# Kernel tuning notes

Hardware: AMD Instinct MI355X
Metric: run time of the kernel (lower is better)

The kernel has to match this reference:

```python
import jax, jax.numpy as jnp
import numpy as np

DIM = 768
N_HEADS = 12
HEAD_DIM = DIM // N_HEADS
SCALE = HEAD_DIM ** -0.5


def setup_inputs() -> dict:
    key = jax.random.key(0)
    kx, kqkv, kpw, kpb = jax.random.split(key, 4)
    B, N = 16, 1024
    x = jax.random.normal(kx, (B, N, DIM), dtype=jnp.float32)
    # nn.Linear weights stored [out, in]; torch computes x @ W.T + b
    w_qkv = jax.random.normal(kqkv, (3 * DIM, DIM), dtype=jnp.float32) * (DIM ** -0.5)
    w_proj = jax.random.normal(kpw, (DIM, DIM), dtype=jnp.float32) * (DIM ** -0.5)
    b_proj = jax.random.normal(kpb, (DIM,), dtype=jnp.float32) * 0.01
    return {"x": x, "w_qkv": w_qkv, "w_proj": w_proj, "b_proj": b_proj}


def reference(x, w_qkv, w_proj, b_proj):
    B, N, C = x.shape
    # qkv: [B, N, 3C] -> [3, B, H, N, Dh]
    qkv = (x @ w_qkv.T).reshape(B, N, 3, N_HEADS, HEAD_DIM)
    qkv = jnp.transpose(qkv, (2, 0, 3, 1, 4))
    q, k, v = qkv[0], qkv[1], qkv[2]
    # scores: [B, H, N, N]
    scores = jnp.einsum("bhnd,bhmd->bhnm", q, k) * SCALE
    attn = jax.nn.softmax(scores, axis=-1)
    out = jnp.einsum("bhnm,bhmd->bhnd", attn, v)
    out = jnp.transpose(out, (0, 2, 1, 3)).reshape(B, N, C)
    return out @ w_proj.T + b_proj
```

## Files before the change

kernel.cpp:

```cpp
#include <hip/hip_runtime.h>
#include <stdint.h>


typedef unsigned short u16;
typedef __attribute__((ext_vector_type(8))) short s16x8;
typedef __attribute__((ext_vector_type(4))) float f32x4;
typedef __attribute__((ext_vector_type(4))) unsigned short u16x4;

#define SEQ 1024
#define NHEAD 12
#define HD 64

__device__ __forceinline__ u16 f2bf(float f) {
  union { float f; uint32_t u; } v; v.f = f;
  uint32_t u = v.u;
  return (u16)((u + 0x7FFFu + ((u >> 16) & 1u)) >> 16);
}

__device__ __forceinline__ float exp2_fast(float x) {
  return __builtin_amdgcn_exp2f(x);
}

__device__ __forceinline__ uint32_t pk_bf16(float a, float b) {
#if __has_builtin(__builtin_amdgcn_cvt_pk_bf16_f32)
  typedef __attribute__((ext_vector_type(2))) __bf16 bf2;
  union { bf2 v; uint32_t u; } c;
  c.v = __builtin_amdgcn_cvt_pk_bf16_f32(a, b);
  return c.u;
#else
  union { float f; uint32_t u; } ua, ub; ua.f = a; ub.f = b;
  const uint32_t ra = ua.u + 0x8000u, rb = ub.u + 0x8000u;
  return __builtin_amdgcn_perm(ra, rb, 0x03020706u);
#endif
}

__device__ __forceinline__ void gld_lds16(const void* g, void* l) {
  __builtin_amdgcn_global_load_lds((const __attribute__((address_space(1))) void*)g,
                                   (__attribute__((address_space(3))) void*)l, 16, 0, 0);
}

__global__ void cvt_bf16(const float* __restrict__ in, u16* __restrict__ out, int n4) {
  int i = blockIdx.x * blockDim.x + threadIdx.x;
  if (i < n4) {
    float4 f = ((const float4*)in)[i];
    u16x4 o;
    o.x = f2bf(f.x); o.y = f2bf(f.y); o.z = f2bf(f.z); o.w = f2bf(f.w);
    ((u16x4*)out)[i] = o;
  }
}

template <int EPI>
__global__ __launch_bounds__(256, 3)
void gemm_bt(const u16* __restrict__ A, const u16* __restrict__ B,
             u16* __restrict__ q, u16* __restrict__ k, u16* __restrict__ v,
             float* __restrict__ out, const float* __restrict__ bias) {
  __shared__ u16 As[128 * 64];
  __shared__ u16 Bs[128 * 64];
  const int tid = threadIdx.x;
  const int wv = tid >> 6, lane = tid & 63;
  const int quad = lane >> 4, l16 = lane & 15;
  const int m0 = blockIdx.x * 128, n0 = blockIdx.y * 128;
  const int wm = (wv & 1) * 64, wn = (wv >> 1) * 64;

  f32x4 acc[4][4];
#pragma unroll
  for (int i = 0; i < 4; i++)
#pragma unroll
    for (int j = 0; j < 4; j++) { acc[i][j].x = 0.f; acc[i][j].y = 0.f; acc[i][j].z = 0.f; acc[i][j].w = 0.f; }

  const int srow = (lane >> 3);
  const int scp = lane & 7;

  for (int kt = 0; kt < 768; kt += 64) {
    __syncthreads();
#pragma unroll
    for (int i = 0; i < 4; i++) {
      const int t = wv * 4 + i;
      const int row = t * 8 + srow;
      const int c = scp ^ (row & 7);
      gld_lds16(A + (size_t)(m0 + row) * 768 + kt + c * 8, &As[t * 512]);
      gld_lds16(B + (size_t)(n0 + row) * 768 + kt + c * 8, &Bs[t * 512]);
    }
    __syncthreads();
#pragma unroll
    for (int ks = 0; ks < 2; ks++) {
      s16x8 af[4], bf[4];
#pragma unroll
      for (int mi = 0; mi < 4; mi++) {
        const int ra = wm + mi * 16 + l16;
        const int ca = ((ks * 4 + quad) ^ (ra & 7)) * 8;
        af[mi] = *(const s16x8*)&As[ra * 64 + ca];
        const int rb = wn + mi * 16 + l16;
        const int cb = ((ks * 4 + quad) ^ (rb & 7)) * 8;
        bf[mi] = *(const s16x8*)&Bs[rb * 64 + cb];
      }
#pragma unroll
      for (int mi = 0; mi < 4; mi++)
#pragma unroll
        for (int ni = 0; ni < 4; ni++)
          acc[mi][ni] = __builtin_amdgcn_mfma_f32_16x16x32_bf16(af[mi], bf[ni], acc[mi][ni], 0, 0, 0);
    }
  }

#pragma unroll
  for (int mi = 0; mi < 4; mi++) {
#pragma unroll
    for (int ni = 0; ni < 4; ni++) {
#pragma unroll
      for (int r = 0; r < 4; r++) {
        const int m = m0 + wm + mi * 16 + quad * 4 + r;
        const int n = n0 + wn + ni * 16 + l16;
        const float val = acc[mi][ni][r];
        if (EPI == 0) {
          const int which = n / 768;
          const int rc = n % 768;
          const int head = rc >> 6, d = rc & 63;
          const int b = m >> 10, rr = m & 1023;
          if (which == 0)
            q[((size_t)(b * NHEAD + head) * SEQ + rr) * HD + d] = f2bf(val * 0.18033688011112042f);
          else if (which == 1)
            k[((size_t)(b * NHEAD + head) * SEQ + rr) * HD + d] = f2bf(val);
          else
            v[((size_t)(b * NHEAD + head) * HD + d) * SEQ + rr] = f2bf(val);
        } else {
          out[(size_t)m * 768 + n] = val + bias[n];
        }
      }
    }
  }
}

__global__ __launch_bounds__(256, 3)
void flash_attn(const u16* __restrict__ Q, const u16* __restrict__ K,
                const u16* __restrict__ VT, u16* __restrict__ O) {
  __shared__ u16 Ks[2][64 * 64];
  __shared__ u16 Vs[2][64 * 64];
  __shared__ u16 Ps[4][32 * 64];

  const int tid = threadIdx.x;
  const int wv = tid >> 6, lane = tid & 63;
  const int quad = lane >> 4, l16 = lane & 15;
  const int bh = blockIdx.x;
  const int q0 = blockIdx.y * 128 + wv * 32;
  const size_t base = (size_t)bh * SEQ * HD;
  const size_t vbase = (size_t)bh * HD * SEQ;
  u16* pw = Ps[wv];

  const int sr0 = tid >> 3;
  const int sc0 = (tid & 7) ^ (sr0 & 7);
  const int sr1 = 32 + sr0;
  const int sc1 = (tid & 7) ^ (sr1 & 7);

  s16x8 qf[2][2];
#pragma unroll
  for (int g = 0; g < 2; g++)
#pragma unroll
    for (int ks = 0; ks < 2; ks++)
      qf[g][ks] = *(const s16x8*)(Q + base + (size_t)(q0 + g * 16 + l16) * HD + ks * 32 + quad * 8);

  const s16x8 ones = {0x3F80, 0x3F80, 0x3F80, 0x3F80, 0x3F80, 0x3F80, 0x3F80, 0x3F80};

  f32x4 acc[2][4], acc_l[2];
#pragma unroll
  for (int g = 0; g < 2; g++) {
    acc_l[g].x = 0.f; acc_l[g].y = 0.f; acc_l[g].z = 0.f; acc_l[g].w = 0.f;
#pragma unroll
    for (int t = 0; t < 4; t++) { acc[g][t].x = 0.f; acc[g][t].y = 0.f; acc[g][t].z = 0.f; acc[g][t].w = 0.f; }
  }

  const int swz = l16 & 7;

  gld_lds16(K + base + (size_t)sr0 * HD + sc0 * 8, &Ks[0][wv * 512]);
  gld_lds16(VT + vbase + (size_t)sr0 * SEQ + sc0 * 8, &Vs[0][wv * 512]);
  gld_lds16(K + base + (size_t)sr1 * HD + sc1 * 8, &Ks[0][2048 + wv * 512]);
  gld_lds16(VT + vbase + (size_t)sr1 * SEQ + sc1 * 8, &Vs[0][2048 + wv * 512]);

  for (int it = 0; it < 16; it++) {
    __syncthreads();
    if (it + 1 < 16) {
      const int n1 = (it + 1) * 64;
      const int nb = (it + 1) & 1;
      gld_lds16(K + base + (size_t)(n1 + sr0) * HD + sc0 * 8, &Ks[nb][wv * 512]);
      gld_lds16(VT + vbase + (size_t)sr0 * SEQ + n1 + sc0 * 8, &Vs[nb][wv * 512]);
      gld_lds16(K + base + (size_t)(n1 + sr1) * HD + sc1 * 8, &Ks[nb][2048 + wv * 512]);
      gld_lds16(VT + vbase + (size_t)sr1 * SEQ + n1 + sc1 * 8, &Vs[nb][2048 + wv * 512]);
    }
    const u16* __restrict__ ks = Ks[it & 1];
    const u16* __restrict__ vs = Vs[it & 1];

    f32x4 s0[4], s1[4];
#pragma unroll
    for (int t = 0; t < 4; t++) {
      s0[t].x = 0.f; s0[t].y = 0.f; s0[t].z = 0.f; s0[t].w = 0.f;
      s1[t].x = 0.f; s1[t].y = 0.f; s1[t].z = 0.f; s1[t].w = 0.f;
      const u16* kr = &ks[(t * 16 + l16) * 64];
      const s16x8 kf0 = *(const s16x8*)&kr[(quad ^ swz) * 8];
      const s16x8 kf1 = *(const s16x8*)&kr[((4 + quad) ^ swz) * 8];
      s0[t] = __builtin_amdgcn_mfma_f32_16x16x32_bf16(kf0, qf[0][0], s0[t], 0, 0, 0);
      s0[t] = __builtin_amdgcn_mfma_f32_16x16x32_bf16(kf1, qf[0][1], s0[t], 0, 0, 0);
      s1[t] = __builtin_amdgcn_mfma_f32_16x16x32_bf16(kf0, qf[1][0], s1[t], 0, 0, 0);
      s1[t] = __builtin_amdgcn_mfma_f32_16x16x32_bf16(kf1, qf[1][1], s1[t], 0, 0, 0);
    }

#pragma unroll
    for (int t = 0; t < 4; t++)
#pragma unroll
      for (int r = 0; r < 4; r++) {
        s0[t][r] = exp2_fast(s0[t][r]);
        s1[t][r] = exp2_fast(s1[t][r]);
      }

#pragma unroll
    for (int t = 0; t < 4; t++) {
      const int p = (2 * t + (quad >> 1)) ^ swz;
      *(uint2*)&pw[l16 * 64 + p * 8 + (quad & 1) * 4] =
          make_uint2(pk_bf16(s0[t][0], s0[t][1]), pk_bf16(s0[t][2], s0[t][3]));
      *(uint2*)&pw[(16 + l16) * 64 + p * 8 + (quad & 1) * 4] =
          make_uint2(pk_bf16(s1[t][0], s1[t][1]), pk_bf16(s1[t][2], s1[t][3]));
    }

#pragma unroll
    for (int ks2 = 0; ks2 < 2; ks2++) {
      const int cp = ((ks2 * 4 + quad) ^ swz) * 8;
      const s16x8 pf0 = *(const s16x8*)&pw[l16 * 64 + cp];
      const s16x8 pf1 = *(const s16x8*)&pw[(16 + l16) * 64 + cp];
      acc_l[0] = __builtin_amdgcn_mfma_f32_16x16x32_bf16(pf0, ones, acc_l[0], 0, 0, 0);
      acc_l[1] = __builtin_amdgcn_mfma_f32_16x16x32_bf16(pf1, ones, acc_l[1], 0, 0, 0);
#pragma unroll
      for (int t2 = 0; t2 < 4; t2++) {
        const s16x8 vf = *(const s16x8*)&vs[(t2 * 16 + l16) * 64 + cp];
        acc[0][t2] = __builtin_amdgcn_mfma_f32_16x16x32_bf16(pf0, vf, acc[0][t2], 0, 0, 0);
        acc[1][t2] = __builtin_amdgcn_mfma_f32_16x16x32_bf16(pf1, vf, acc[1][t2], 0, 0, 0);
      }
    }
  }

  const int b = bh / NHEAD, h = bh % NHEAD;
#pragma unroll
  for (int g = 0; g < 2; g++) {
#pragma unroll
    for (int r = 0; r < 4; r++) {
      const float li = 1.0f / acc_l[g][r];
      const int qrow = q0 + g * 16 + quad * 4 + r;
      u16* op = O + (size_t)(b * SEQ + qrow) * 768 + h * HD;
#pragma unroll
      for (int t2 = 0; t2 < 4; t2++)
        op[t2 * 16 + l16] = f2bf(acc[g][t2][r] * li);
    }
  }
}

extern "C" void kernel_launch(void* const* d_in, const int* in_sizes, int n_in,
                              void* d_out, int out_size, void* d_ws, size_t ws_size,
                              hipStream_t stream) {
  (void)in_sizes; (void)n_in; (void)out_size; (void)ws_size;
  const float* x      = (const float*)d_in[0];
  const float* w_qkv  = (const float*)d_in[1];
  const float* w_proj = (const float*)d_in[2];
  const float* b_proj = (const float*)d_in[3];

  const size_t SZ_X   = (size_t)16384 * 768;
  const size_t SZ_WQ  = (size_t)2304 * 768;
  const size_t SZ_WP  = (size_t)768 * 768;
  const size_t SZ_HED = (size_t)16 * NHEAD * SEQ * HD;

  u16* xb   = (u16*)d_ws;
  u16* wqb  = xb + SZ_X;
  u16* wpb  = wqb + SZ_WQ;
  u16* qb   = wpb + SZ_WP;
  u16* kb   = qb + SZ_HED;
  u16* vtb  = kb + SZ_HED;
  u16* attn = vtb + SZ_HED;

  cvt_bf16<<<(int)(SZ_X / 4 / 256), 256, 0, stream>>>(x, xb, (int)(SZ_X / 4));
  cvt_bf16<<<(int)(SZ_WQ / 4 / 256), 256, 0, stream>>>(w_qkv, wqb, (int)(SZ_WQ / 4));
  cvt_bf16<<<(int)(SZ_WP / 4 / 256), 256, 0, stream>>>(w_proj, wpb, (int)(SZ_WP / 4));

  gemm_bt<0><<<dim3(128, 18), 256, 0, stream>>>(xb, wqb, qb, kb, vtb, nullptr, nullptr);
  flash_attn<<<dim3(192, 8), 256, 0, stream>>>(qb, kb, vtb, attn);
  gemm_bt<1><<<dim3(128, 6), 256, 0, stream>>>(attn, wpb, nullptr, nullptr, nullptr,
                                               (float*)d_out, b_proj);
}
```

Before: 298.2 us.

## Rewrite GEMM with 256x256 tiles, double-buffered LDS pipeline and grid swizzle

The QKV and output-projection GEMMs now use 512-thread blocks computing 256x256 tiles. Global-to-LDS loads are double-buffered and interleaved with four MFMA phases per k-step, using explicit barriers, waitcnt and priority hints. Block IDs are swizzled for L2 locality. The aim is to hide load latency and raise data reuse per tile, at the cost of more LDS (128KB), more registers and fewer blocks, which hurts wave-count balance across CUs.

Result: slower. 328.9 us (+10.3%).

```diff
diff --git a/kernel.cpp b/kernel.cpp
--- a/kernel.cpp
+++ b/kernel.cpp
@@ -39,6 +39,14 @@
                                    (__attribute__((address_space(3))) void*)l, 16, 0, 0);
 }
 
+__device__ __forceinline__ void phase_bar() {
+  __builtin_amdgcn_sched_barrier(0);
+  asm volatile("" ::: "memory");
+  __builtin_amdgcn_s_barrier();
+  asm volatile("" ::: "memory");
+  __builtin_amdgcn_sched_barrier(0);
+}
+
 __global__ void cvt_bf16(const float* __restrict__ in, u16* __restrict__ out, int n4) {
   int i = blockIdx.x * blockDim.x + threadIdx.x;
   if (i < n4) {
@@ -50,84 +58,170 @@
 }
 
 template <int EPI>
-__global__ __launch_bounds__(256, 3)
+__global__ __launch_bounds__(512, 2)
 void gemm_bt(const u16* __restrict__ A, const u16* __restrict__ B,
              u16* __restrict__ q, u16* __restrict__ k, u16* __restrict__ v,
              float* __restrict__ out, const float* __restrict__ bias) {
-  __shared__ u16 As[128 * 64];
-  __shared__ u16 Bs[128 * 64];
+  __shared__ u16 As[2][256 * 64];
+  __shared__ u16 Bs[2][256 * 64];
+  constexpr int NTN = (EPI == 0) ? 9 : 3;
+  constexpr int NWG = 64 * NTN;
+  constexpr int CPX = NWG / 8;
+
   const int tid = threadIdx.x;
   const int wv = tid >> 6, lane = tid & 63;
   const int quad = lane >> 4, l16 = lane & 15;
-  const int m0 = blockIdx.x * 128, n0 = blockIdx.y * 128;
-  const int wm = (wv & 1) * 64, wn = (wv >> 1) * 64;
-
-  f32x4 acc[4][4];
-#pragma unroll
-  for (int i = 0; i < 4; i++)
+  const int bid = blockIdx.x;
+  const int swz = (bid & 7) * CPX + (bid >> 3);
+  const int m0 = (swz / NTN) * 256;
+  const int n0 = (swz % NTN) * 256;
+  const int wm = (wv >> 2) * 128, wn = (wv & 3) * 64;
+  const int srow = tid >> 3, slot = tid & 7;
+
+#define STAGE_A(bufi, kt, half)                                              \
+  do {                                                                       \
+    _Pragma("unroll")                                                        \
+    for (int j = 0; j < 2; j++) {                                            \
+      const int row_ = (half) * 128 + j * 64 + srow;                         \
+      const int c_ = slot ^ (row_ & 7);                                      \
+      gld_lds16(A + (size_t)(m0 + row_) * 768 + (kt) + c_ * 8,               \
+                &As[bufi][((half) * 128 + j * 64 + wv * 8) * 64]);           \
+    }                                                                        \
+  } while (0)
+
+#define STAGE_B(bufi, kt, half)                                              \
+  do {                                                                       \
+    _Pragma("unroll")                                                        \
+    for (int j = 0; j < 2; j++) {                                            \
+      const int row_ = (half) * 128 + j * 64 + srow;                         \
+      const int c_ = slot ^ (row_ & 7);                                      \
+      gld_lds16(B + (size_t)(n0 + row_) * 768 + (kt) + c_ * 8,               \
+                &Bs[bufi][((half) * 128 + j * 64 + wv * 8) * 64]);           \
+    }                                                                        \
+  } while (0)
+
+#define READ_A(qd)                                                           \
+  do {                                                                       \
+    _Pragma("unroll")                                                        \
+    for (int i = 0; i < 2; i++) {                                            \
+      const int ra_ = wm + ((qd) * 2 + i) * 16 + l16;                        \
+      _Pragma("unroll")                                                      \
+      for (int ks = 0; ks < 2; ks++)                                         \
+        af[i][ks] = *(const s16x8*)&As[buf][ra_ * 64 + (((ks * 4 + quad) ^ (ra_ & 7)) * 8)]; \
+    }                                                                        \
+  } while (0)
+
+#define READ_B()                                                             \
+  do {                                                                       \
+    _Pragma("unroll")                                                        \
+    for (int ni = 0; ni < 4; ni++) {                                         \
+      const int rb_ = wn + ni * 16 + l16;                                    \
+      _Pragma("unroll")                                                      \
+      for (int ks = 0; ks < 2; ks++)                                         \
+        bf[ks][ni] = *(const s16x8*)&Bs[buf][rb_ * 64 + (((ks * 4 + quad) ^ (rb_ & 7)) * 8)]; \
+    }                                                                        \
+  } while (0)
+
+#define MFMA_Q(qd)                                                           \
+  do {                                                                       \
+    __builtin_amdgcn_s_setprio(1);                                           \
+    _Pragma("unroll")                                                        \
+    for (int i = 0; i < 2; i++)                                              \
+      _Pragma("unroll")                                                      \
+      for (int ni = 0; ni < 4; ni++) {                                       \
+        acc[(qd) * 2 + i][ni] = __builtin_amdgcn_mfma_f32_16x16x32_bf16(     \
+            af[i][0], bf[0][ni], acc[(qd) * 2 + i][ni], 0, 0, 0);            \
+        acc[(qd) * 2 + i][ni] = __builtin_amdgcn_mfma_f32_16x16x32_bf16(     \
+            af[i][1], bf[1][ni], acc[(qd) * 2 + i][ni], 0, 0, 0);            \
+      }                                                                      \
+    __builtin_amdgcn_s_setprio(0);                                           \
+  } while (0)
+
+  f32x4 acc[8][4];
+#pragma unroll
+  for (int i = 0; i < 8; i++)
 #pragma unroll
     for (int j = 0; j < 4; j++) { acc[i][j].x = 0.f; acc[i][j].y = 0.f; acc[i][j].z = 0.f; acc[i][j].w = 0.f; }
 
-  const int srow = (lane >> 3);
-  const int scp = lane & 7;
-
-  for (int kt = 0; kt < 768; kt += 64) {
-    __syncthreads();
-#pragma unroll
-    for (int i = 0; i < 4; i++) {
-      const int t = wv * 4 + i;
-      const int row = t * 8 + srow;
-      const int c = scp ^ (row & 7);
-      gld_lds16(A + (size_t)(m0 + row) * 768 + kt + c * 8, &As[t * 512]);
-      gld_lds16(B + (size_t)(n0 + row) * 768 + kt + c * 8, &Bs[t * 512]);
-    }
-    __syncthreads();
-#pragma unroll
-    for (int ks = 0; ks < 2; ks++) {
-      s16x8 af[4], bf[4];
-#pragma unroll
-      for (int mi = 0; mi < 4; mi++) {
-        const int ra = wm + mi * 16 + l16;
-        const int ca = ((ks * 4 + quad) ^ (ra & 7)) * 8;
-        af[mi] = *(const s16x8*)&As[ra * 64 + ca];
-        const int rb = wn + mi * 16 + l16;
-        const int cb = ((ks * 4 + quad) ^ (rb & 7)) * 8;
-        bf[mi] = *(const s16x8*)&Bs[rb * 64 + cb];
-      }
-#pragma unroll
-      for (int mi = 0; mi < 4; mi++)
-#pragma unroll
-        for (int ni = 0; ni < 4; ni++)
-          acc[mi][ni] = __builtin_amdgcn_mfma_f32_16x16x32_bf16(af[mi], bf[ni], acc[mi][ni], 0, 0, 0);
-    }
-  }
-
-#pragma unroll
-  for (int mi = 0; mi < 4; mi++) {
+  STAGE_A(0, 0, 0); STAGE_A(0, 0, 1);
+  STAGE_B(0, 0, 0); STAGE_B(0, 0, 1);
+  STAGE_B(1, 64, 0);
+  asm volatile("s_waitcnt vmcnt(2)" ::: "memory");
+  phase_bar();
+
+  for (int t = 0; t < 12; t++) {
+    const int buf = t & 1;
+    const int ktn = (t + 1) * 64;
+    s16x8 af[2][2], bf[2][4];
+
+    READ_B();
+    READ_A(0);
+    if (t < 11) STAGE_A(buf ^ 1, ktn, 0);
+    phase_bar();
+    MFMA_Q(0);
+    phase_bar();
+
+    READ_A(1);
+    if (t < 11) STAGE_A(buf ^ 1, ktn, 1);
+    phase_bar();
+    MFMA_Q(1);
+    phase_bar();
+
+    READ_A(2);
+    if (t < 11) STAGE_B(buf ^ 1, ktn, 1);
+    phase_bar();
+    MFMA_Q(2);
+    phase_bar();
+
+    READ_A(3);
+    if (t < 10) STAGE_B(buf, ktn + 64, 0);
+    phase_bar();
+    MFMA_Q(3);
+    if (t < 10) { asm volatile("s_waitcnt vmcnt(2)" ::: "memory"); }
+    else        { asm volatile("s_waitcnt vmcnt(0)" ::: "memory"); }
+    phase_bar();
+  }
+
+  if (EPI == 0) {
 #pragma unroll
     for (int ni = 0; ni < 4; ni++) {
-#pragma unroll
-      for (int r = 0; r < 4; r++) {
-        const int m = m0 + wm + mi * 16 + quad * 4 + r;
-        const int n = n0 + wn + ni * 16 + l16;
-        const float val = acc[mi][ni][r];
-        if (EPI == 0) {
-          const int which = n / 768;
-          const int rc = n % 768;
-          const int head = rc >> 6, d = rc & 63;
+      const int n = n0 + wn + ni * 16 + l16;
+      const int which = n / 768;
+      const int rc = n % 768;
+      const int head = rc >> 6, d = rc & 63;
+#pragma unroll
+      for (int mi = 0; mi < 8; mi++) {
+#pragma unroll
+        for (int r = 0; r < 4; r++) {
+          const int m = m0 + wm + mi * 16 + quad * 4 + r;
           const int b = m >> 10, rr = m & 1023;
+          const float val = acc[mi][ni][r];
           if (which == 0)
             q[((size_t)(b * NHEAD + head) * SEQ + rr) * HD + d] = f2bf(val * 0.18033688011112042f);
           else if (which == 1)
             k[((size_t)(b * NHEAD + head) * SEQ + rr) * HD + d] = f2bf(val);
           else
             v[((size_t)(b * NHEAD + head) * HD + d) * SEQ + rr] = f2bf(val);
-        } else {
-          out[(size_t)m * 768 + n] = val + bias[n];
         }
       }
     }
-  }
+  } else {
+#pragma unroll
+    for (int mi = 0; mi < 8; mi++)
+#pragma unroll
+      for (int ni = 0; ni < 4; ni++)
+#pragma unroll
+        for (int r = 0; r < 4; r++) {
+          const int m = m0 + wm + mi * 16 + quad * 4 + r;
+          const int n = n0 + wn + ni * 16 + l16;
+          out[(size_t)m * 768 + n] = acc[mi][ni][r] + bias[n];
+        }
+  }
+#undef STAGE_A
+#undef STAGE_B
+#undef READ_A
+#undef READ_B
+#undef MFMA_Q
 }
 
 __global__ __launch_bounds__(256, 3)
@@ -276,8 +370,8 @@
   cvt_bf16<<<(int)(SZ_WQ / 4 / 256), 256, 0, stream>>>(w_qkv, wqb, (int)(SZ_WQ / 4));
   cvt_bf16<<<(int)(SZ_WP / 4 / 256), 256, 0, stream>>>(w_proj, wpb, (int)(SZ_WP / 4));
 
-  gemm_bt<0><<<dim3(128, 18), 256, 0, stream>>>(xb, wqb, qb, kb, vtb, nullptr, nullptr);
+  gemm_bt<0><<<dim3(576), 512, 0, stream>>>(xb, wqb, qb, kb, vtb, nullptr, nullptr);
   flash_attn<<<dim3(192, 8), 256, 0, stream>>>(qb, kb, vtb, attn);
-  gemm_bt<1><<<dim3(128, 6), 256, 0, stream>>>(attn, wpb, nullptr, nullptr, nullptr,
-                                               (float*)d_out, b_proj);
-}
+  gemm_bt<1><<<dim3(192), 512, 0, stream>>>(attn, wpb, nullptr, nullptr, nullptr,
+                                            (float*)d_out, b_proj);
+}
```
